# Kernel tuning notes

Hardware: AMD Instinct MI355X
Metric: run time of the kernel (lower is better)

The kernel has to match this reference:

```python
import jax, jax.numpy as jnp
import numpy as np

MX, SX = 0.0, 1.0  # msx
MY, SY = 0.0, 1.0  # msy


def _mode_linear(inp, phase, w, b):
    # Equivalent to: w_p = einsum('ji,imk->jmk', phase, w); out = squeeze(inp[:,None,:] @ w_p) + phase @ b
    # Fused blended form avoids the (batch, in, out) per-sample weight intermediate.
    out = jnp.einsum('bd,idh,bi->bh', inp, w, phase)
    return out + phase @ b


def setup_inputs() -> dict:
    key = jax.random.key(0)
    ks = jax.random.split(key, 4)
    B, D_IN, H, D_OUT = 32768, 256, 1024, 64
    x = jax.random.normal(ks[0], (B, D_IN + 2), dtype=jnp.float32)
    w1 = jax.random.normal(ks[1], (2, D_IN, H), dtype=jnp.float32) * 0.05
    b1 = jnp.zeros((2, H), dtype=jnp.float32)
    w2 = jax.random.normal(ks[2], (2, H, H), dtype=jnp.float32) * 0.05
    b2 = jnp.zeros((2, H), dtype=jnp.float32)
    w3 = jax.random.normal(ks[3], (2, H, D_OUT), dtype=jnp.float32) * 0.05
    b3 = jnp.zeros((2, D_OUT), dtype=jnp.float32)
    return {"x": x, "w1": w1, "b1": b1, "w2": w2, "b2": b2, "w3": w3, "b3": b3}


def reference(x, w1, b1, w2, b2, w3, b3):
    phase = x[:, -2:]                 # unscaled phase weights, per original code
    xs = (x - MX) / SX
    h = xs[:, :-2]                    # [B, D_IN]
    out = jax.nn.elu(_mode_linear(h, phase, w1, b1))
    out = jax.nn.elu(_mode_linear(out, phase, w2, b2))
    out = _mode_linear(out, phase, w3, b3)
    return out * SY + MY
```

## Files before the change

### kernel.cpp

```cpp
#include <hip/hip_runtime.h>

typedef unsigned short u16;
typedef __bf16 bf16x8 __attribute__((ext_vector_type(8)));
typedef float f32x4 __attribute__((ext_vector_type(4)));
typedef float f32x16 __attribute__((ext_vector_type(16)));

#define AS1 __attribute__((address_space(1)))
#define AS3 __attribute__((address_space(3)))

static __device__ __forceinline__ u16 f2bf(float f) {
  union { float f; unsigned u; } v; v.f = f;
  unsigned r = (v.u + 0x7fff + ((v.u >> 16) & 1)) >> 16;
  return (u16)r;
}

__global__ void prep_x_kernel(const float* __restrict__ x, u16* __restrict__ hx,
                              float2* __restrict__ phase, int B) {
  int i = blockIdx.x * blockDim.x + threadIdx.x;
  int total = B * 128;
  if (i < total) {
    int row = i >> 7, k2 = (i & 127);
    const float2 v = *reinterpret_cast<const float2*>(x + (size_t)row * 258 + k2 * 2);
    u16 a = f2bf(v.x), b = f2bf(v.y);
    *reinterpret_cast<unsigned*>(hx + (size_t)row * 256 + k2 * 2) =
        (unsigned)a | ((unsigned)b << 16);
  }
  if (i < B) {
    phase[i] = *reinterpret_cast<const float2*>(x + (size_t)i * 258 + 256);
  }
}

__global__ void prep_w_kernel(const float* __restrict__ w, u16* __restrict__ wt,
                              int K, int N) {
  __shared__ u16 tile[64][65];
  int k0 = blockIdx.x * 64, n0 = blockIdx.y * 64, mode = blockIdx.z;
  const float* src = w + (size_t)mode * K * N;
  u16* dst = wt + (size_t)mode * N * K;
  int c = threadIdx.x & 63;
  int r4 = threadIdx.x >> 6;
#pragma unroll
  for (int i = 0; i < 16; ++i) {
    int r = r4 + i * 4;
    tile[r][c] = f2bf(src[(size_t)(k0 + r) * N + n0 + c]);
  }
  __syncthreads();
#pragma unroll
  for (int i = 0; i < 16; ++i) {
    int r = r4 + i * 4;
    dst[(size_t)(n0 + r) * K + k0 + c] = tile[c][r];
  }
}

__global__ void prep_w_int_kernel(const float* __restrict__ w, u16* __restrict__ wt,
                                  int K, int N) {
  __shared__ u16 tile[64][65];
  int k0 = blockIdx.x * 64, n0 = blockIdx.y * 64, mode = blockIdx.z;
  const float* src = w + (size_t)mode * K * N;
  int c = threadIdx.x & 63;
  int r4 = threadIdx.x >> 6;
#pragma unroll
  for (int i = 0; i < 16; ++i) {
    int r = r4 + i * 4;
    tile[r][c] = f2bf(src[(size_t)(k0 + r) * N + n0 + c]);
  }
  __syncthreads();
#pragma unroll
  for (int i = 0; i < 16; ++i) {
    int n = n0 + r4 + i * 4;
    int np = ((n >> 5) << 6) + (mode << 5) + (n & 31);
    wt[(size_t)np * K + k0 + c] = tile[c][r4 + i * 4];
  }
}

template <bool ELU_STORE>
__global__ __launch_bounds__(512, 2) void gemm_ring32(
    const u16* __restrict__ A, const u16* __restrict__ Wt,
    const float* __restrict__ bias, const float2* __restrict__ phase,
    u16* __restrict__ out, int K, int Np) {
  __shared__ u16 lds[4][2][8192];
  const int tnc = Np >> 8;
  const int nwg = gridDim.x;
  int id = blockIdx.x;
  const int cpx = nwg >> 3;
  id = (id & 7) * cpx + (id >> 3);
  const int m0 = (id / tnc) * 256;
  const int n0 = (id % tnc) * 256;
  const int t = threadIdx.x;
  const int lane = t & 63;
  const int wave = t >> 6;
  const int wr = wave >> 2, wc = wave & 3;
  const int l31 = lane & 31, lhi = lane >> 5;

  const int sub_l = ((l31 >> 4) & 1) * 1024 + (l31 & 15) * 64;
  int cx[2];
#pragma unroll
  for (int kk = 0; kk < 2; ++kk)
    cx[kk] = (((kk * 16 + lhi * 8) ^ (((l31 >> 3) & 1) << 4)) << 1);

  int soff[2];
#pragma unroll
  for (int ld = 0; ld < 2; ++ld) {
    int e = (ld * 512 + t) * 8;
    int st = e >> 9;
    int rl = (e >> 5) & 15;
    int c = e & 31;
    int c0 = c ^ (((rl >> 3) & 1) << 4);
    soff[ld] = (st * 16 + rl) * K + c0;
  }
  const u16* Abase = A + (size_t)m0 * K;
  const u16* Bbase = Wt + (size_t)n0 * K;

  f32x16 acc[4][2] = {};
  const int NT = K >> 5;

  auto stage = [&](int bb, int tile) {
    const int kt = tile << 5;
#pragma unroll
    for (int ld = 0; ld < 2; ++ld)
      __builtin_amdgcn_global_load_lds(
          (const AS1 void*)(Abase + kt + soff[ld]),
          (AS3 void*)(&lds[bb][0][(ld * 512 + t) * 8]), 16, 0, 0);
#pragma unroll
    for (int ld = 0; ld < 2; ++ld)
      __builtin_amdgcn_global_load_lds(
          (const AS1 void*)(Bbase + kt + soff[ld]),
          (AS3 void*)(&lds[bb][1][(ld * 512 + t) * 8]), 16, 0, 0);
  };

#define BAR()                    \
  asm volatile("" ::: "memory"); \
  __builtin_amdgcn_s_barrier();  \
  asm volatile("" ::: "memory");

#define LOADA(mh)                                                            \
  _Pragma("unroll") for (int m = 0; m < 2; ++m)                              \
  _Pragma("unroll") for (int kk = 0; kk < 2; ++kk)                           \
      af[m][kk] = *(const bf16x8*)(lA +                                      \
          ((wr * 8 + ((mh)*2 + m) * 2) << 10) + sub_l + cx[kk]);
#define LOADB()                                                              \
  _Pragma("unroll") for (int n = 0; n < 2; ++n)                              \
  _Pragma("unroll") for (int kk = 0; kk < 2; ++kk)                           \
      bfr[n][kk] = *(const bf16x8*)(lB +                                     \
          ((wc * 4 + n * 2) << 10) + sub_l + cx[kk]);
#define MFMAH(mh)                                                            \
  __builtin_amdgcn_s_setprio(1);                                             \
  _Pragma("unroll") for (int m = 0; m < 2; ++m)                              \
  _Pragma("unroll") for (int n = 0; n < 2; ++n)                              \
  _Pragma("unroll") for (int kk = 0; kk < 2; ++kk)                           \
      acc[(mh)*2 + m][n] = __builtin_amdgcn_mfma_f32_32x32x16_bf16(          \
          af[m][kk], bfr[n][kk], acc[(mh)*2 + m][n], 0, 0, 0);               \
  __builtin_amdgcn_s_setprio(0);

  stage(0, 0);
  stage(1, 1);
  stage(2, 2);
  asm volatile("s_waitcnt vmcnt(8)" ::: "memory");
  BAR();

  for (int tt = 0; tt < NT; ++tt) {
    const char* lA = (const char*)&lds[tt & 3][0][0];
    const char* lB = (const char*)&lds[tt & 3][1][0];
    bf16x8 af[2][2], bfr[2][2];
    LOADA(0);
    LOADB();
    if (tt + 3 < NT) stage((tt + 3) & 3, tt + 3);
    BAR();
    MFMAH(0);
    BAR();
    LOADA(1);
    BAR();
    MFMAH(1);
    asm volatile("s_waitcnt vmcnt(8)" ::: "memory");
    BAR();
  }
#undef LOADA
#undef LOADB
#undef MFMAH

  const int Nreal = Np >> 1;
  const int col = (n0 >> 1) + wc * 32 + l31;
  const float bias0 = bias[col];
  const float bias1 = bias[Nreal + col];
#pragma unroll
  for (int m = 0; m < 4; ++m) {
#pragma unroll
    for (int rg = 0; rg < 16; ++rg) {
      int grow = m0 + wr * 128 + m * 32 + (rg & 3) + 8 * (rg >> 2) + 4 * lhi;
      float2 ph = phase[grow];
      float v = ph.x * (acc[m][0][rg] + bias0) + ph.y * (acc[m][1][rg] + bias1);
      if (ELU_STORE) v = v > 0.f ? v : (__expf(v) - 1.f);
      out[(size_t)grow * Nreal + col] = f2bf(v);
    }
  }
#undef BAR
}

template <int BM, int BN, int WM, int WN, bool ELU_BF16>
__launch_bounds__(256, 2) __global__
void gemm_dualmode(const u16* __restrict__ A, const u16* __restrict__ WT,
                   const float* __restrict__ bias, const float2* __restrict__ phase,
                   void* __restrict__ out, int K, int N) {
  constexpr int MF = WM / 16, NF = WN / 16;
  __shared__ u16 ldsA[BM * 32];
  __shared__ u16 ldsB[2][BN * 32];
  const int m0 = blockIdx.x * BM;
  const int n0 = blockIdx.y * BN;
  const int t = threadIdx.x;
  const int wave = t >> 6, lane = t & 63;
  constexpr int NWC = BN / WN;
  const int wr = wave / NWC, wc = wave % NWC;
  const int lr = lane & 15, ks = lane >> 4;

  f32x4 acc[2][MF][NF] = {};

  for (int kt = 0; kt < K; kt += 32) {
#pragma unroll
    for (int i = 0; i < BM / 64; ++i) {
      int tt = t + i * 256;
      int r = tt >> 2, c8 = (tt & 3) * 8;
      __builtin_amdgcn_global_load_lds(
          (const AS1 void*)(A + (size_t)(m0 + r) * K + kt + c8),
          (AS3 void*)(ldsA + (size_t)tt * 8), 16, 0, 0);
    }
#pragma unroll
    for (int md = 0; md < 2; ++md) {
#pragma unroll
      for (int i = 0; i < BN / 64; ++i) {
        int tt = t + i * 256;
        int r = tt >> 2, c8 = (tt & 3) * 8;
        __builtin_amdgcn_global_load_lds(
            (const AS1 void*)(WT + (size_t)md * N * K + (size_t)(n0 + r) * K + kt + c8),
            (AS3 void*)(ldsB[md] + (size_t)tt * 8), 16, 0, 0);
      }
    }
    __syncthreads();

    bf16x8 af[MF], b0f[NF], b1f[NF];
#pragma unroll
    for (int m = 0; m < MF; ++m)
      af[m] = *reinterpret_cast<const bf16x8*>(&ldsA[(wr * WM + m * 16 + lr) * 32 + ks * 8]);
#pragma unroll
    for (int n = 0; n < NF; ++n) {
      b0f[n] = *reinterpret_cast<const bf16x8*>(&ldsB[0][(wc * WN + n * 16 + lr) * 32 + ks * 8]);
      b1f[n] = *reinterpret_cast<const bf16x8*>(&ldsB[1][(wc * WN + n * 16 + lr) * 32 + ks * 8]);
    }
#pragma unroll
    for (int m = 0; m < MF; ++m) {
#pragma unroll
      for (int n = 0; n < NF; ++n) {
        acc[0][m][n] = __builtin_amdgcn_mfma_f32_16x16x32_bf16(af[m], b0f[n], acc[0][m][n], 0, 0, 0);
        acc[1][m][n] = __builtin_amdgcn_mfma_f32_16x16x32_bf16(af[m], b1f[n], acc[1][m][n], 0, 0, 0);
      }
    }
    __syncthreads();
  }

#pragma unroll
  for (int m = 0; m < MF; ++m) {
#pragma unroll
    for (int j = 0; j < 4; ++j) {
      int grow = m0 + wr * WM + m * 16 + ks * 4 + j;
      float2 ph = phase[grow];
#pragma unroll
      for (int n = 0; n < NF; ++n) {
        int gcol = n0 + wc * WN + n * 16 + lr;
        float v = ph.x * (acc[0][m][n][j] + bias[gcol]) +
                  ph.y * (acc[1][m][n][j] + bias[N + gcol]);
        if (ELU_BF16) {
          v = v > 0.f ? v : (__expf(v) - 1.f);
          ((u16*)out)[(size_t)grow * N + gcol] = f2bf(v);
        } else {
          ((float*)out)[(size_t)grow * N + gcol] = v;
        }
      }
    }
  }
}

extern "C" void kernel_launch(void* const* d_in, const int* in_sizes, int n_in,
                              void* d_out, int out_size, void* d_ws, size_t ws_size,
                              hipStream_t stream) {
  const float* x  = (const float*)d_in[0];
  const float* w1 = (const float*)d_in[1];
  const float* b1 = (const float*)d_in[2];
  const float* w2 = (const float*)d_in[3];
  const float* b2 = (const float*)d_in[4];
  const float* w3 = (const float*)d_in[5];
  const float* b3 = (const float*)d_in[6];
  float* out = (float*)d_out;
  const int B = 32768, DIN = 256, H = 1024, DOUT = 64;

  char* ws = (char*)d_ws;
  u16* W1Ti = (u16*)ws;    ws += (size_t)2 * H * DIN * 2;
  u16* W2Ti = (u16*)ws;    ws += (size_t)2 * H * H * 2;
  u16* W3T = (u16*)ws;     ws += (size_t)2 * DOUT * H * 2;
  float2* phase = (float2*)ws; ws += (size_t)B * 8;
  u16* hx = (u16*)ws;      ws += (size_t)B * DIN * 2;
  u16* h1 = (u16*)ws;      ws += (size_t)B * H * 2;
  u16* h2 = (u16*)ws;      ws += (size_t)B * H * 2;

  prep_x_kernel<<<(B * 128 + 255) / 256, 256, 0, stream>>>(x, hx, phase, B);
  prep_w_int_kernel<<<dim3(DIN / 64, H / 64, 2), 256, 0, stream>>>(w1, W1Ti, DIN, H);
  prep_w_int_kernel<<<dim3(H / 64, H / 64, 2), 256, 0, stream>>>(w2, W2Ti, H, H);
  prep_w_kernel<<<dim3(H / 64, DOUT / 64, 2), 256, 0, stream>>>(w3, W3T, H, DOUT);

  const int nwg = (B / 256) * (2 * H / 256);
  gemm_ring32<true><<<nwg, 512, 0, stream>>>(hx, W1Ti, b1, phase, h1, DIN, 2 * H);
  gemm_ring32<true><<<nwg, 512, 0, stream>>>(h1, W2Ti, b2, phase, h2, H, 2 * H);
  gemm_dualmode<128, 64, 64, 32, false>
      <<<dim3(B / 128, DOUT / 64), 256, 0, stream>>>(h2, W3T, b3, phase, out, H, DOUT);
}
```

Measured before the change: 263.6 us.

## Software-pipeline LDS fragment loads and change swizzle in ring GEMM

Restructures the main loop of the ring-buffered GEMM so A/B fragments for the next tile are loaded from LDS right after the barrier and the second A half is loaded while the first MFMA batch runs. This cuts the per-iteration barriers from four to one. It also replaces the LDS XOR swizzle with a 4-way 16-byte-chunk pattern, intended to reduce bank conflicts on ds_read. The cost is more live fragment registers, and correctness now depends on the single barrier plus the vmcnt waits ordering the ring buffer reuse.

```diff
diff --git a/kernel.cpp b/kernel.cpp
--- a/kernel.cpp
+++ b/kernel.cpp
@@ -51,8 +51,8 @@
   }
 }
 
-__global__ void prep_w_int_kernel(const float* __restrict__ w, u16* __restrict__ wt,
-                                  int K, int N) {
+__global__ void prep_w_int32_kernel(const float* __restrict__ w, u16* __restrict__ wt,
+                                    int K, int N) {
   __shared__ u16 tile[64][65];
   int k0 = blockIdx.x * 64, n0 = blockIdx.y * 64, mode = blockIdx.z;
   const float* src = w + (size_t)mode * K * N;
@@ -90,22 +90,21 @@
   const int wave = t >> 6;
   const int wr = wave >> 2, wc = wave & 3;
   const int l31 = lane & 31, lhi = lane >> 5;
-
-  const int sub_l = ((l31 >> 4) & 1) * 1024 + (l31 & 15) * 64;
-  int cx[2];
+  const int rl = lane & 15;
+
+  int cx32[2];
 #pragma unroll
   for (int kk = 0; kk < 2; ++kk)
-    cx[kk] = (((kk * 16 + lhi * 8) ^ (((l31 >> 3) & 1) << 4)) << 1);
+    cx32[kk] = ((l31 >> 4) << 10) + rl * 64 +
+               ((((kk * 2 + lhi) ^ ((rl >> 1) & 3))) << 4);
 
   int soff[2];
 #pragma unroll
   for (int ld = 0; ld < 2; ++ld) {
-    int e = (ld * 512 + t) * 8;
-    int st = e >> 9;
-    int rl = (e >> 5) & 15;
-    int c = e & 31;
-    int c0 = c ^ (((rl >> 3) & 1) << 4);
-    soff[ld] = (st * 16 + rl) * K + c0;
+    int e = (ld * 512 + t) * 16;
+    int st = e >> 10, rr = (e >> 6) & 15, sp = (e >> 4) & 3;
+    int s = sp ^ ((rr >> 1) & 3);
+    soff[ld] = (st * 16 + rr) * K + s * 8;
   }
   const u16* Abase = A + (size_t)m0 * K;
   const u16* Bbase = Wt + (size_t)n0 * K;
@@ -132,48 +131,60 @@
   __builtin_amdgcn_s_barrier();  \
   asm volatile("" ::: "memory");
 
-#define LOADA(mh)                                                            \
-  _Pragma("unroll") for (int m = 0; m < 2; ++m)                              \
-  _Pragma("unroll") for (int kk = 0; kk < 2; ++kk)                           \
-      af[m][kk] = *(const bf16x8*)(lA +                                      \
-          ((wr * 8 + ((mh)*2 + m) * 2) << 10) + sub_l + cx[kk]);
-#define LOADB()                                                              \
-  _Pragma("unroll") for (int n = 0; n < 2; ++n)                              \
-  _Pragma("unroll") for (int kk = 0; kk < 2; ++kk)                           \
-      bfr[n][kk] = *(const bf16x8*)(lB +                                     \
-          ((wc * 4 + n * 2) << 10) + sub_l + cx[kk]);
-#define MFMAH(mh)                                                            \
-  __builtin_amdgcn_s_setprio(1);                                             \
-  _Pragma("unroll") for (int m = 0; m < 2; ++m)                              \
-  _Pragma("unroll") for (int n = 0; n < 2; ++n)                              \
-  _Pragma("unroll") for (int kk = 0; kk < 2; ++kk)                           \
-      acc[(mh)*2 + m][n] = __builtin_amdgcn_mfma_f32_32x32x16_bf16(          \
-          af[m][kk], bfr[n][kk], acc[(mh)*2 + m][n], 0, 0, 0);               \
+#define LOADA0(buf)                                                           \
+  _Pragma("unroll") for (int m = 0; m < 2; ++m)                               \
+  _Pragma("unroll") for (int kk = 0; kk < 2; ++kk)                            \
+      af0[m][kk] = *(const bf16x8*)((const char*)&lds[buf][0][0] +            \
+                                    ((wr * 8 + m * 2) << 10) + cx32[kk]);
+#define LOADA1(buf)                                                           \
+  _Pragma("unroll") for (int m = 0; m < 2; ++m)                               \
+  _Pragma("unroll") for (int kk = 0; kk < 2; ++kk)                            \
+      af1[m][kk] = *(const bf16x8*)((const char*)&lds[buf][0][0] +            \
+                                    ((wr * 8 + (m + 2) * 2) << 10) + cx32[kk]);
+#define LOADB(buf)                                                            \
+  _Pragma("unroll") for (int n = 0; n < 2; ++n)                               \
+  _Pragma("unroll") for (int kk = 0; kk < 2; ++kk)                            \
+      bfr[n][kk] = *(const bf16x8*)((const char*)&lds[buf][1][0] +            \
+                                    ((wc * 4 + n * 2) << 10) + cx32[kk]);
+#define MFMAH(mh, AF)                                                         \
+  __builtin_amdgcn_s_setprio(1);                                              \
+  _Pragma("unroll") for (int m = 0; m < 2; ++m)                               \
+  _Pragma("unroll") for (int n = 0; n < 2; ++n)                               \
+  _Pragma("unroll") for (int kk = 0; kk < 2; ++kk)                            \
+      acc[(mh)*2 + m][n] = __builtin_amdgcn_mfma_f32_32x32x16_bf16(           \
+          AF[m][kk], bfr[n][kk], acc[(mh)*2 + m][n], 0, 0, 0);                \
   __builtin_amdgcn_s_setprio(0);
+
+  bf16x8 af0[2][2], af1[2][2], bfr[2][2];
 
   stage(0, 0);
   stage(1, 1);
   stage(2, 2);
   asm volatile("s_waitcnt vmcnt(8)" ::: "memory");
   BAR();
+  LOADA0(0);
+  LOADB(0);
 
   for (int tt = 0; tt < NT; ++tt) {
-    const char* lA = (const char*)&lds[tt & 3][0][0];
-    const char* lB = (const char*)&lds[tt & 3][1][0];
-    bf16x8 af[2][2], bfr[2][2];
-    LOADA(0);
-    LOADB();
-    if (tt + 3 < NT) stage((tt + 3) & 3, tt + 3);
+    const int b = tt & 3;
+    LOADA1(b);
+    MFMAH(0, af0);
+    if (tt + 3 < NT) {
+      stage((tt + 3) & 3, tt + 3);
+      asm volatile("s_waitcnt vmcnt(8)" ::: "memory");
+    } else {
+      asm volatile("s_waitcnt vmcnt(0)" ::: "memory");
+    }
+    MFMAH(1, af1);
     BAR();
-    MFMAH(0);
-    BAR();
-    LOADA(1);
-    BAR();
-    MFMAH(1);
-    asm volatile("s_waitcnt vmcnt(8)" ::: "memory");
-    BAR();
-  }
-#undef LOADA
+    if (tt + 1 < NT) {
+      const int b2 = (tt + 1) & 3;
+      LOADA0(b2);
+      LOADB(b2);
+    }
+  }
+#undef LOADA0
+#undef LOADA1
 #undef LOADB
 #undef MFMAH
 
@@ -300,8 +311,8 @@
   u16* h2 = (u16*)ws;      ws += (size_t)B * H * 2;
 
   prep_x_kernel<<<(B * 128 + 255) / 256, 256, 0, stream>>>(x, hx, phase, B);
-  prep_w_int_kernel<<<dim3(DIN / 64, H / 64, 2), 256, 0, stream>>>(w1, W1Ti, DIN, H);
-  prep_w_int_kernel<<<dim3(H / 64, H / 64, 2), 256, 0, stream>>>(w2, W2Ti, H, H);
+  prep_w_int32_kernel<<<dim3(DIN / 64, H / 64, 2), 256, 0, stream>>>(w1, W1Ti, DIN, H);
+  prep_w_int32_kernel<<<dim3(H / 64, H / 64, 2), 256, 0, stream>>>(w2, W2Ti, H, H);
   prep_w_kernel<<<dim3(H / 64, DOUT / 64, 2), 256, 0, stream>>>(w3, W3T, H, DOUT);
 
   const int nwg = (B / 256) * (2 * H / 256);
```

Measured after the change: 254.2 us. 3.6% less time.
